# Kernel tuning notes

Measured on AMD Instinct MI355X. Metric: run time of the kernel, lower is better.

Reference implementation:

```python
import jax, jax.numpy as jnp
import numpy as np


def _logcumsumexp(x, axis):
    return jax.lax.associative_scan(jnp.logaddexp, x, axis=axis)


def _log_g(x):
    # log of g(x) = where(x>=0, x+0.5, sigmoid(x))
    return jnp.where(x >= 0, jnp.log(jax.nn.relu(x) + 0.5), -jax.nn.softplus(-x))


def _min_gru(x, Wz, bz, Wh, bh):
    # x: [B, S, D_in] -> h: [B, S, H]; log-space Heinsen parallel scan over S
    k = x @ Wz + bz                      # gate pre-activation
    log_z = -jax.nn.softplus(-k)         # log(sigmoid(k))  = log z
    log_coeffs = -jax.nn.softplus(k)     # log(1 - sigmoid(k))
    log_tilde_h = _log_g(x @ Wh + bh)    # log candidate hidden
    a_star = jnp.cumsum(log_coeffs, axis=1)
    log_h = a_star + _logcumsumexp(log_z + log_tilde_h - a_star, axis=1)
    return jnp.exp(log_h)


def setup_inputs() -> dict:
    key = jax.random.key(0)
    ks = jax.random.split(key, 7)
    B, S, D, H = 4, 4096, 1024, 1024
    s_in = 1.0 / np.sqrt(D)
    s_cat = 1.0 / np.sqrt(2 * H)
    return {
        "x": jax.random.normal(ks[0], (B, S, D), jnp.float32),
        "Wz_f": jax.random.normal(ks[1], (D, H), jnp.float32) * s_in,
        "bz_f": jnp.zeros((H,), jnp.float32),
        "Wh_f": jax.random.normal(ks[2], (D, H), jnp.float32) * s_in,
        "bh_f": jnp.zeros((H,), jnp.float32),
        "Wz_b": jax.random.normal(ks[3], (D, H), jnp.float32) * s_in,
        "bz_b": jnp.zeros((H,), jnp.float32),
        "Wh_b": jax.random.normal(ks[4], (D, H), jnp.float32) * s_in,
        "bh_b": jnp.zeros((H,), jnp.float32),
        "W_out": jax.random.normal(ks[5], (2 * H, H), jnp.float32) * s_cat,
        "b_out": jnp.zeros((H,), jnp.float32),
    }


def reference(x, Wz_f, bz_f, Wh_f, bh_f, Wz_b, bz_b, Wh_b, bh_b, W_out, b_out):
    x_rev = jnp.flip(x, axis=1)
    out_fwd = _min_gru(x, Wz_f, bz_f, Wh_f, bh_f)        # [B, S, H]
    out_bwd = _min_gru(x_rev, Wz_b, bz_b, Wh_b, bh_b)    # [B, S, H] (not re-flipped, per source)
    concat = jnp.concatenate([out_fwd, out_bwd], axis=2)  # [B, S, 2H]
    return concat @ W_out + b_out                         # [B, S, H]
```

## Files before the change

### kernel.cpp

```cpp
#include <hip/hip_runtime.h>
#include <stdint.h>

typedef __attribute__((ext_vector_type(8))) short bf16x8;
typedef __attribute__((ext_vector_type(4))) float f32x4;

#define SEQ 4096

__device__ __forceinline__ float bf2f(unsigned short u) {
  union { unsigned int i; float f; } v; v.i = ((unsigned int)u) << 16; return v.f;
}
__device__ __forceinline__ unsigned short f2bf(float f) {
  union { float f; unsigned int i; } v; v.f = f;
  unsigned int u = v.i;
  u = u + 0x7FFFu + ((u >> 16) & 1u);
  return (unsigned short)(u >> 16);
}
__device__ __forceinline__ float sigm(float x) { return 1.0f / (1.0f + __expf(-x)); }


__global__ void cvt_x_kernel(const float* __restrict__ in, unsigned short* __restrict__ out, int n8) {
  int i = blockIdx.x * blockDim.x + threadIdx.x;
  int stride = gridDim.x * blockDim.x;
  for (; i < n8; i += stride) {
    const float4* p = (const float4*)in + (size_t)i * 2;
    float4 a = p[0], b = p[1];
    union { unsigned short u[8]; uint4 v; } r;
    r.u[0] = f2bf(a.x); r.u[1] = f2bf(a.y); r.u[2] = f2bf(a.z); r.u[3] = f2bf(a.w);
    r.u[4] = f2bf(b.x); r.u[5] = f2bf(b.y); r.u[6] = f2bf(b.z); r.u[7] = f2bf(b.w);
    ((uint4*)out)[i] = r.v;
  }
}

__global__ void tconv32_kernel(const float* __restrict__ src, unsigned short* __restrict__ dst,
                               int K, int N) {
  __shared__ float t[32][33];
  int n0 = blockIdx.x * 32, k0 = blockIdx.y * 32;
  int tx = threadIdx.x & 31, ty = threadIdx.x >> 5;
#pragma unroll
  for (int i = 0; i < 32; i += 8)
    t[ty + i][tx] = src[(size_t)(k0 + ty + i) * N + n0 + tx];
  __syncthreads();
#pragma unroll
  for (int i = 0; i < 32; i += 8)
    dst[(size_t)(n0 + ty + i) * K + k0 + tx] = f2bf(t[tx][ty + i]);
}

__global__ void concat_bias_kernel(const float* b0, const float* b1, const float* b2,
                                   const float* b3, float* b4) {
  int i = blockIdx.x * 256 + threadIdx.x;
  const float* p = (i < 1024) ? b0 : (i < 2048) ? b1 : (i < 3072) ? b2 : b3;
  b4[i] = p[i & 1023];
}


template <int MODE>
__global__ __launch_bounds__(512, 2) void gemm256_kernel(
    const unsigned short* __restrict__ A, const unsigned short* __restrict__ BT,
    const float* __restrict__ bias, void* __restrict__ Cout, int K, int NT) {
  __shared__ unsigned short lds[32768];

  const int tid = threadIdx.x;
  const int lane = tid & 63;
  const int wv = tid >> 6;
  const int wm = wv >> 2;
  const int wn = wv & 3;
  const int lo = lane & 15, hi = lane >> 4;

  const int nwg = gridDim.x;
  const int bid = blockIdx.x;
  const int cpx = nwg >> 3;
  const int sw = (bid & 7) * cpx + (bid >> 3);
  const int mt = sw / NT, nt = sw - mt * NT;
  const int m0 = mt << 8, n0 = nt << 8;

  const int srow = tid >> 2;
  const int skb = (((tid & 3) ^ ((tid >> 3) & 3)) << 4);
  const unsigned short* pA0 = A + (size_t)(m0 + srow) * K + (skb >> 1);
  const unsigned short* pA1 = pA0 + (size_t)128 * K;
  const unsigned short* pB0 = BT + (size_t)(n0 + srow) * K + (skb >> 1);
  const unsigned short* pB1 = pB0 + (size_t)128 * K;
  const int dstBase = wv << 9;

#define GLL(SRC, DIDX)                                                                  \
  __builtin_amdgcn_global_load_lds((const __attribute__((address_space(1))) void*)(SRC), \
                                   (__attribute__((address_space(3))) void*)&lds[DIDX], \
                                   16, 0, 0)
#define STAGE(KT, BUF)                                   \
  do {                                                   \
    const int ko_ = (KT) << 5;                           \
    GLL(pA0 + ko_, (BUF) * 8192 + dstBase);              \
    GLL(pA1 + ko_, (BUF) * 8192 + 4096 + dstBase);       \
    GLL(pB0 + ko_, 16384 + (BUF) * 8192 + dstBase);      \
    GLL(pB1 + ko_, 16384 + (BUF) * 8192 + 4096 + dstBase); \
  } while (0)

  f32x4 acc[8][4];
#pragma unroll
  for (int i = 0; i < 8; ++i)
#pragma unroll
    for (int j = 0; j < 4; ++j) acc[i][j] = (f32x4){0.f, 0.f, 0.f, 0.f};

  const int swz = ((lo >> 1) & 3) << 4;
  const int kof = ((hi << 4) ^ swz) >> 1;
  const int aRow = wm * 128 + lo;
  const int bRow = wn * 64 + lo;

  const int nT = K >> 5;
  STAGE(0, 0);
  for (int kt = 0; kt < nT; ++kt) {
    const int buf = kt & 1;
    if (kt + 1 < nT) {
      STAGE(kt + 1, buf ^ 1);
      asm volatile("s_waitcnt vmcnt(4)" ::: "memory");
    } else {
      asm volatile("s_waitcnt vmcnt(0)" ::: "memory");
    }
    __builtin_amdgcn_s_barrier();
    const int aOff = buf * 8192;
    const int bOff = 16384 + buf * 8192;

    bf16x8 af[8];
#pragma unroll
    for (int mi = 0; mi < 8; ++mi)
      af[mi] = *(const bf16x8*)&lds[aOff + (aRow + mi * 16) * 32 + kof];
    bf16x8 b0 = *(const bf16x8*)&lds[bOff + (bRow + 0) * 32 + kof];
    bf16x8 b1 = *(const bf16x8*)&lds[bOff + (bRow + 16) * 32 + kof];
    __builtin_amdgcn_s_setprio(1);
#pragma unroll
    for (int mi = 0; mi < 8; ++mi) {
      acc[mi][0] = __builtin_amdgcn_mfma_f32_16x16x32_bf16(af[mi], b0, acc[mi][0], 0, 0, 0);
      acc[mi][1] = __builtin_amdgcn_mfma_f32_16x16x32_bf16(af[mi], b1, acc[mi][1], 0, 0, 0);
    }
    __builtin_amdgcn_s_setprio(0);
    __builtin_amdgcn_s_barrier();

    bf16x8 b2 = *(const bf16x8*)&lds[bOff + (bRow + 32) * 32 + kof];
    bf16x8 b3 = *(const bf16x8*)&lds[bOff + (bRow + 48) * 32 + kof];
    __builtin_amdgcn_s_setprio(1);
#pragma unroll
    for (int mi = 0; mi < 8; ++mi) {
      acc[mi][2] = __builtin_amdgcn_mfma_f32_16x16x32_bf16(af[mi], b2, acc[mi][2], 0, 0, 0);
      acc[mi][3] = __builtin_amdgcn_mfma_f32_16x16x32_bf16(af[mi], b3, acc[mi][3], 0, 0, 0);
    }
    __builtin_amdgcn_s_setprio(0);
    asm volatile("s_waitcnt lgkmcnt(0)" ::: "memory");
    __builtin_amdgcn_s_barrier();
  }
#undef STAGE
#undef GLL

#pragma unroll
  for (int mi = 0; mi < 8; ++mi) {
#pragma unroll
    for (int ni = 0; ni < 4; ++ni) {
      int col = n0 + wn * 64 + ni * 16 + lo;
      int rb = m0 + wm * 128 + mi * 16 + hi * 4;
      float bcol = bias[col];
      f32x4 v = acc[mi][ni];
      if (MODE == 0) {
        unsigned short* ACTp = (unsigned short*)Cout;
        bool isz = ((col >> 10) & 1) == 0;
#pragma unroll
        for (int r = 0; r < 4; ++r) {
          float x = v[r] + bcol;
          float res;
          if (isz) res = sigm(-x);
          else res = (x >= 0.f) ? (x + 0.5f) : sigm(x);
          ACTp[(size_t)(rb + r) * 4096 + col] = f2bf(res);
        }
      } else {
        float* Op = (float*)Cout;
#pragma unroll
        for (int r = 0; r < 4; ++r) Op[(size_t)(rb + r) * 1024 + col] = v[r] + bcol;
      }
    }
  }
}


__global__ __launch_bounds__(256) void scan_phase1_kernel(const unsigned short* __restrict__ ACT,
                                                          float* __restrict__ CHA,
                                                          float* __restrict__ CHB) {
  int tid = threadIdx.x;
  int cb = blockIdx.x & 3;
  int chunk = (blockIdx.x >> 2) & 31;
  int b = (blockIdx.x >> 7) & 3;
  int dir = (blockIdx.x >> 9) & 1;
  int c = cb * 256 + tid;
  int t0 = chunk * 128;
  size_t colA = (size_t)dir * 2048 + c;
  float Ap = 1.f, Bv = 0.f;
  for (int i = 0; i < 128; ++i) {
    int t = t0 + i;
    int s = dir ? (SEQ - 1 - t) : t;
    size_t base = ((size_t)b * SEQ + s) * 4096;
    float a = bf2f(ACT[base + colA]);
    float g = bf2f(ACT[base + colA + 1024]);
    Bv = a * Bv + (1.f - a) * g;
    Ap *= a;
  }
  size_t o = ((size_t)(dir * 4 + b) * 32 + chunk) * 1024 + c;
  CHA[o] = Ap;
  CHB[o] = Bv;
}

__global__ __launch_bounds__(256) void scan_phase2_kernel(const float* __restrict__ CHA,
                                                          const float* __restrict__ CHB,
                                                          float* __restrict__ HINIT) {
  int idx = blockIdx.x * 256 + threadIdx.x;
  int c = idx & 1023;
  int db = idx >> 10;
  float h = 0.f;
  for (int ck = 0; ck < 32; ++ck) {
    size_t o = ((size_t)db * 32 + ck) * 1024 + c;
    HINIT[o] = h;
    h = CHA[o] * h + CHB[o];
  }
}

__global__ __launch_bounds__(256) void scan_phase3_kernel(const unsigned short* __restrict__ ACT,
                                                          const float* __restrict__ HINIT,
                                                          unsigned short* __restrict__ HCAT) {
  int tid = threadIdx.x;
  int cb = blockIdx.x & 3;
  int chunk = (blockIdx.x >> 2) & 31;
  int b = (blockIdx.x >> 7) & 3;
  int dir = (blockIdx.x >> 9) & 1;
  int c = cb * 256 + tid;
  int t0 = chunk * 128;
  size_t colA = (size_t)dir * 2048 + c;
  float h = HINIT[((size_t)(dir * 4 + b) * 32 + chunk) * 1024 + c];
  for (int i = 0; i < 128; ++i) {
    int t = t0 + i;
    int s = dir ? (SEQ - 1 - t) : t;
    size_t base = ((size_t)b * SEQ + s) * 4096;
    float a = bf2f(ACT[base + colA]);
    float g = bf2f(ACT[base + colA + 1024]);
    h = a * h + (1.f - a) * g;
    HCAT[((size_t)b * SEQ + t) * 2048 + dir * 1024 + c] = f2bf(h);
  }
}


extern "C" void kernel_launch(void* const* d_in, const int* in_sizes, int n_in,
                              void* d_out, int out_size, void* d_ws, size_t ws_size,
                              hipStream_t stream) {
  (void)in_sizes; (void)n_in; (void)out_size; (void)ws_size;
  const float* x     = (const float*)d_in[0];
  const float* Wz_f  = (const float*)d_in[1];
  const float* bz_f  = (const float*)d_in[2];
  const float* Wh_f  = (const float*)d_in[3];
  const float* bh_f  = (const float*)d_in[4];
  const float* Wz_b  = (const float*)d_in[5];
  const float* bz_b  = (const float*)d_in[6];
  const float* Wh_b  = (const float*)d_in[7];
  const float* bh_b  = (const float*)d_in[8];
  const float* W_out = (const float*)d_in[9];
  const float* b_out = (const float*)d_in[10];

  char* ws = (char*)d_ws;
  size_t off = 0;
  auto alloc = [&](size_t bytes) {
    char* p = ws + off;
    off = (off + bytes + 255) & ~(size_t)255;
    return p;
  };
  const size_t M = 16384;
  unsigned short* xb    = (unsigned short*)alloc(M * 1024 * 2);
  unsigned short* WT4   = (unsigned short*)alloc(4096ull * 1024 * 2);
  unsigned short* WTout = (unsigned short*)alloc(1024ull * 2048 * 2);
  unsigned short* ACT   = (unsigned short*)alloc(M * 4096 * 2);
  unsigned short* HCAT  = (unsigned short*)alloc(M * 2048 * 2);
  float* CHA   = (float*)alloc(262144ull * 4);
  float* CHB   = (float*)alloc(262144ull * 4);
  float* HINIT = (float*)alloc(262144ull * 4);
  float* b4    = (float*)alloc(4096 * 4);

  cvt_x_kernel<<<2048, 256, 0, stream>>>(x, xb, (int)(M * 1024 / 8));

  tconv32_kernel<<<dim3(32, 32), 256, 0, stream>>>(Wz_f, WT4 + 0 * 1048576, 1024, 1024);
  tconv32_kernel<<<dim3(32, 32), 256, 0, stream>>>(Wh_f, WT4 + 1 * 1048576, 1024, 1024);
  tconv32_kernel<<<dim3(32, 32), 256, 0, stream>>>(Wz_b, WT4 + 2 * 1048576, 1024, 1024);
  tconv32_kernel<<<dim3(32, 32), 256, 0, stream>>>(Wh_b, WT4 + 3 * 1048576, 1024, 1024);
  tconv32_kernel<<<dim3(32, 64), 256, 0, stream>>>(W_out, WTout, 2048, 1024);
  concat_bias_kernel<<<16, 256, 0, stream>>>(bz_f, bh_f, bz_b, bh_b, b4);

  gemm256_kernel<0><<<1024, 512, 0, stream>>>(xb, WT4, b4, (void*)ACT, 1024, 16);

  scan_phase1_kernel<<<1024, 256, 0, stream>>>(ACT, CHA, CHB);
  scan_phase2_kernel<<<32, 256, 0, stream>>>(CHA, CHB, HINIT);
  scan_phase3_kernel<<<1024, 256, 0, stream>>>(ACT, HINIT, HCAT);

  gemm256_kernel<1><<<256, 512, 0, stream>>>(HCAT, WTout, b_out, d_out, 2048, 4);
}
```

Baseline: 337.8 us.

## Merge weight transposes, split gate GEMM with BK64 variant, vectorize scan kernels

The five weight-transpose launches become one 3D-grid launch. The first GEMM is split into two half-N launches: one keeps the original BK=32 kernel and the other uses a new BK=64 variant with a 128KB LDS double buffer. The scan phases 1 and 3 now process 4 channels per thread with vector loads and stores, and the chunk count goes from 32 to 64 with shorter chunks. This cuts launch overhead and uncoalesced narrow scan accesses. The 128KB LDS kernel limits occupancy to one block per CU, and splitting the GEMM leaves a partial wave at its tail.

```diff
diff --git a/kernel.cpp b/kernel.cpp
--- a/kernel.cpp
+++ b/kernel.cpp
@@ -3,6 +3,7 @@
 
 typedef __attribute__((ext_vector_type(8))) short bf16x8;
 typedef __attribute__((ext_vector_type(4))) float f32x4;
+typedef __attribute__((ext_vector_type(4))) unsigned short u16x4;
 
 #define SEQ 4096
 
@@ -31,14 +32,24 @@
   }
 }
 
-__global__ void tconv32_kernel(const float* __restrict__ src, unsigned short* __restrict__ dst,
-                               int K, int N) {
+__global__ void tconvb_kernel(const float* __restrict__ s0, const float* __restrict__ s1,
+                              const float* __restrict__ s2, const float* __restrict__ s3,
+                              const float* __restrict__ s4, unsigned short* __restrict__ WT4,
+                              unsigned short* __restrict__ WTout) {
   __shared__ float t[32][33];
-  int n0 = blockIdx.x * 32, k0 = blockIdx.y * 32;
+  int z = blockIdx.z;
+  const float* src; unsigned short* dst; int K, k0;
+  if (z < 4) {
+    src = (z == 0) ? s0 : (z == 1) ? s1 : (z == 2) ? s2 : s3;
+    dst = WT4 + (size_t)z * 1048576; K = 1024; k0 = blockIdx.y * 32;
+  } else {
+    src = s4; dst = WTout; K = 2048; k0 = blockIdx.y * 32 + (z - 4) * 1024;
+  }
+  int n0 = blockIdx.x * 32;
   int tx = threadIdx.x & 31, ty = threadIdx.x >> 5;
 #pragma unroll
   for (int i = 0; i < 32; i += 8)
-    t[ty + i][tx] = src[(size_t)(k0 + ty + i) * N + n0 + tx];
+    t[ty + i][tx] = src[(size_t)(k0 + ty + i) * 1024 + n0 + tx];
   __syncthreads();
 #pragma unroll
   for (int i = 0; i < 32; i += 8)
@@ -52,11 +63,42 @@
   b4[i] = p[i & 1023];
 }
 
+template <int MODE>
+__device__ __forceinline__ void gemm_epilogue(f32x4 (&acc)[8][4], const float* bias,
+                                              void* Cout, int m0, int n0, int wm, int wn,
+                                              int lo, int hi) {
+#pragma unroll
+  for (int mi = 0; mi < 8; ++mi) {
+#pragma unroll
+    for (int ni = 0; ni < 4; ++ni) {
+      int col = n0 + wn * 64 + ni * 16 + lo;
+      int rb = m0 + wm * 128 + mi * 16 + hi * 4;
+      float bcol = bias[col];
+      f32x4 v = acc[mi][ni];
+      if (MODE == 0) {
+        unsigned short* ACTp = (unsigned short*)Cout;
+        bool isz = ((col >> 10) & 1) == 0;
+#pragma unroll
+        for (int r = 0; r < 4; ++r) {
+          float x = v[r] + bcol;
+          float res;
+          if (isz) res = sigm(-x);
+          else res = (x >= 0.f) ? (x + 0.5f) : sigm(x);
+          ACTp[(size_t)(rb + r) * 4096 + col] = f2bf(res);
+        }
+      } else {
+        float* Op = (float*)Cout;
+#pragma unroll
+        for (int r = 0; r < 4; ++r) Op[(size_t)(rb + r) * 1024 + col] = v[r] + bcol;
+      }
+    }
+  }
+}
 
 template <int MODE>
 __global__ __launch_bounds__(512, 2) void gemm256_kernel(
     const unsigned short* __restrict__ A, const unsigned short* __restrict__ BT,
-    const float* __restrict__ bias, void* __restrict__ Cout, int K, int NT) {
+    const float* __restrict__ bias, void* __restrict__ Cout, int K, int NT, int ntOff) {
   __shared__ unsigned short lds[32768];
 
   const int tid = threadIdx.x;
@@ -71,7 +113,7 @@
   const int cpx = nwg >> 3;
   const int sw = (bid & 7) * cpx + (bid >> 3);
   const int mt = sw / NT, nt = sw - mt * NT;
-  const int m0 = mt << 8, n0 = nt << 8;
+  const int m0 = mt << 8, n0 = (nt + ntOff) << 8;
 
   const int srow = tid >> 2;
   const int skb = (((tid & 3) ^ ((tid >> 3) & 3)) << 4);
@@ -85,12 +127,12 @@
   __builtin_amdgcn_global_load_lds((const __attribute__((address_space(1))) void*)(SRC), \
                                    (__attribute__((address_space(3))) void*)&lds[DIDX], \
                                    16, 0, 0)
-#define STAGE(KT, BUF)                                   \
-  do {                                                   \
-    const int ko_ = (KT) << 5;                           \
-    GLL(pA0 + ko_, (BUF) * 8192 + dstBase);              \
-    GLL(pA1 + ko_, (BUF) * 8192 + 4096 + dstBase);       \
-    GLL(pB0 + ko_, 16384 + (BUF) * 8192 + dstBase);      \
+#define STAGE(KT, BUF)                                     \
+  do {                                                     \
+    const int ko_ = (KT) << 5;                             \
+    GLL(pA0 + ko_, (BUF) * 8192 + dstBase);                \
+    GLL(pA1 + ko_, (BUF) * 8192 + 4096 + dstBase);         \
+    GLL(pB0 + ko_, 16384 + (BUF) * 8192 + dstBase);        \
     GLL(pB1 + ko_, 16384 + (BUF) * 8192 + 4096 + dstBase); \
   } while (0)
 
@@ -148,60 +190,130 @@
   }
 #undef STAGE
 #undef GLL
-
-#pragma unroll
-  for (int mi = 0; mi < 8; ++mi) {
-#pragma unroll
-    for (int ni = 0; ni < 4; ++ni) {
-      int col = n0 + wn * 64 + ni * 16 + lo;
-      int rb = m0 + wm * 128 + mi * 16 + hi * 4;
-      float bcol = bias[col];
-      f32x4 v = acc[mi][ni];
-      if (MODE == 0) {
-        unsigned short* ACTp = (unsigned short*)Cout;
-        bool isz = ((col >> 10) & 1) == 0;
-#pragma unroll
-        for (int r = 0; r < 4; ++r) {
-          float x = v[r] + bcol;
-          float res;
-          if (isz) res = sigm(-x);
-          else res = (x >= 0.f) ? (x + 0.5f) : sigm(x);
-          ACTp[(size_t)(rb + r) * 4096 + col] = f2bf(res);
-        }
-      } else {
-        float* Op = (float*)Cout;
-#pragma unroll
-        for (int r = 0; r < 4; ++r) Op[(size_t)(rb + r) * 1024 + col] = v[r] + bcol;
-      }
-    }
-  }
-}
-
-
-__global__ __launch_bounds__(256) void scan_phase1_kernel(const unsigned short* __restrict__ ACT,
-                                                          float* __restrict__ CHA,
-                                                          float* __restrict__ CHB) {
-  int tid = threadIdx.x;
-  int cb = blockIdx.x & 3;
-  int chunk = (blockIdx.x >> 2) & 31;
-  int b = (blockIdx.x >> 7) & 3;
-  int dir = (blockIdx.x >> 9) & 1;
-  int c = cb * 256 + tid;
-  int t0 = chunk * 128;
-  size_t colA = (size_t)dir * 2048 + c;
-  float Ap = 1.f, Bv = 0.f;
-  for (int i = 0; i < 128; ++i) {
+  gemm_epilogue<MODE>(acc, bias, Cout, m0, n0, wm, wn, lo, hi);
+}
+
+template <int MODE>
+__global__ __launch_bounds__(512, 2) void gemm256b_kernel(
+    const unsigned short* __restrict__ A, const unsigned short* __restrict__ BT,
+    const float* __restrict__ bias, void* __restrict__ Cout, int K, int NT, int ntOff) {
+  __shared__ unsigned short lds[65536];
+
+  const int tid = threadIdx.x;
+  const int lane = tid & 63;
+  const int wv = tid >> 6;
+  const int wm = wv >> 2;
+  const int wn = wv & 3;
+  const int lo = lane & 15, hi = lane >> 4;
+
+  const int nwg = gridDim.x;
+  const int bid = blockIdx.x;
+  const int cpx = nwg >> 3;
+  const int sw = (bid & 7) * cpx + (bid >> 3);
+  const int mt = sw / NT, nt = sw - mt * NT;
+  const int m0 = mt << 8, n0 = (nt + ntOff) << 8;
+
+  const int srow = tid >> 3;
+  const int skb = (((tid & 7) ^ ((tid >> 3) & 7)) << 4);
+  const unsigned short* pA = A + (size_t)(m0 + srow) * K + (skb >> 1);
+  const unsigned short* pB = BT + (size_t)(n0 + srow) * K + (skb >> 1);
+  const int dstBase = wv << 9;
+
+#define GLLB(SRC, DIDX)                                                                 \
+  __builtin_amdgcn_global_load_lds((const __attribute__((address_space(1))) void*)(SRC), \
+                                   (__attribute__((address_space(3))) void*)&lds[DIDX], \
+                                   16, 0, 0)
+#define STAGEB(KT, BUF)                                          \
+  do {                                                           \
+    const int ko_ = (KT) << 6;                                   \
+    _Pragma("unroll")                                            \
+    for (int j = 0; j < 4; ++j) {                                \
+      GLLB(pA + (size_t)64 * j * K + ko_,                        \
+           (BUF) * 16384 + j * 4096 + dstBase);                  \
+      GLLB(pB + (size_t)64 * j * K + ko_,                        \
+           32768 + (BUF) * 16384 + j * 4096 + dstBase);          \
+    }                                                            \
+  } while (0)
+
+  f32x4 acc[8][4];
+#pragma unroll
+  for (int i = 0; i < 8; ++i)
+#pragma unroll
+    for (int j = 0; j < 4; ++j) acc[i][j] = (f32x4){0.f, 0.f, 0.f, 0.f};
+
+  const int swz8 = (lo & 7) << 4;
+  const int aRow = wm * 128 + lo;
+  const int bRow = wn * 64 + lo;
+
+  const int nT = K >> 6;
+  STAGEB(0, 0);
+  for (int kt = 0; kt < nT; ++kt) {
+    const int buf = kt & 1;
+    if (kt + 1 < nT) {
+      STAGEB(kt + 1, buf ^ 1);
+      asm volatile("s_waitcnt vmcnt(8)" ::: "memory");
+    } else {
+      asm volatile("s_waitcnt vmcnt(0)" ::: "memory");
+    }
+    __builtin_amdgcn_s_barrier();
+    const int aOff = buf * 16384;
+    const int bOff = 32768 + buf * 16384;
+
+#pragma unroll
+    for (int ks = 0; ks < 2; ++ks) {
+      const int kof = ((ks * 64 + hi * 16) ^ swz8) >> 1;
+      bf16x8 af[8], bf[4];
+#pragma unroll
+      for (int mi = 0; mi < 8; ++mi)
+        af[mi] = *(const bf16x8*)&lds[aOff + (aRow + mi * 16) * 64 + kof];
+#pragma unroll
+      for (int ni = 0; ni < 4; ++ni)
+        bf[ni] = *(const bf16x8*)&lds[bOff + (bRow + ni * 16) * 64 + kof];
+      __builtin_amdgcn_s_setprio(1);
+#pragma unroll
+      for (int mi = 0; mi < 8; ++mi)
+#pragma unroll
+        for (int ni = 0; ni < 4; ++ni)
+          acc[mi][ni] = __builtin_amdgcn_mfma_f32_16x16x32_bf16(af[mi], bf[ni],
+                                                                acc[mi][ni], 0, 0, 0);
+      __builtin_amdgcn_s_setprio(0);
+    }
+    asm volatile("s_waitcnt lgkmcnt(0)" ::: "memory");
+    __builtin_amdgcn_s_barrier();
+  }
+#undef STAGEB
+#undef GLLB
+  gemm_epilogue<MODE>(acc, bias, Cout, m0, n0, wm, wn, lo, hi);
+}
+
+
+__global__ __launch_bounds__(256) void scan1v_kernel(const unsigned short* __restrict__ ACT,
+                                                     float* __restrict__ CHA,
+                                                     float* __restrict__ CHB) {
+  int chunk = blockIdx.x & 63;
+  int b = (blockIdx.x >> 6) & 3;
+  int dir = blockIdx.x >> 8;
+  int c4 = threadIdx.x * 4;
+  size_t colA = (size_t)dir * 2048 + c4;
+  float Ap[4] = {1.f, 1.f, 1.f, 1.f};
+  float Bv[4] = {0.f, 0.f, 0.f, 0.f};
+  int t0 = chunk * 64;
+  for (int i = 0; i < 64; ++i) {
     int t = t0 + i;
     int s = dir ? (SEQ - 1 - t) : t;
-    size_t base = ((size_t)b * SEQ + s) * 4096;
-    float a = bf2f(ACT[base + colA]);
-    float g = bf2f(ACT[base + colA + 1024]);
-    Bv = a * Bv + (1.f - a) * g;
-    Ap *= a;
-  }
-  size_t o = ((size_t)(dir * 4 + b) * 32 + chunk) * 1024 + c;
-  CHA[o] = Ap;
-  CHB[o] = Bv;
+    size_t base = ((size_t)b * SEQ + s) * 4096 + colA;
+    u16x4 av = *(const u16x4*)&ACT[base];
+    u16x4 gv = *(const u16x4*)&ACT[base + 1024];
+#pragma unroll
+    for (int j = 0; j < 4; ++j) {
+      float a = bf2f(av[j]), g = bf2f(gv[j]);
+      Bv[j] = a * Bv[j] + (1.f - a) * g;
+      Ap[j] *= a;
+    }
+  }
+  size_t o = ((size_t)(dir * 4 + b) * 64 + chunk) * 1024 + c4;
+  *(float4*)&CHA[o] = (float4){Ap[0], Ap[1], Ap[2], Ap[3]};
+  *(float4*)&CHB[o] = (float4){Bv[0], Bv[1], Bv[2], Bv[3]};
 }
 
 __global__ __launch_bounds__(256) void scan_phase2_kernel(const float* __restrict__ CHA,
@@ -211,33 +323,38 @@
   int c = idx & 1023;
   int db = idx >> 10;
   float h = 0.f;
-  for (int ck = 0; ck < 32; ++ck) {
-    size_t o = ((size_t)db * 32 + ck) * 1024 + c;
+  for (int ck = 0; ck < 64; ++ck) {
+    size_t o = ((size_t)db * 64 + ck) * 1024 + c;
     HINIT[o] = h;
     h = CHA[o] * h + CHB[o];
   }
 }
 
-__global__ __launch_bounds__(256) void scan_phase3_kernel(const unsigned short* __restrict__ ACT,
-                                                          const float* __restrict__ HINIT,
-                                                          unsigned short* __restrict__ HCAT) {
-  int tid = threadIdx.x;
-  int cb = blockIdx.x & 3;
-  int chunk = (blockIdx.x >> 2) & 31;
-  int b = (blockIdx.x >> 7) & 3;
-  int dir = (blockIdx.x >> 9) & 1;
-  int c = cb * 256 + tid;
-  int t0 = chunk * 128;
-  size_t colA = (size_t)dir * 2048 + c;
-  float h = HINIT[((size_t)(dir * 4 + b) * 32 + chunk) * 1024 + c];
-  for (int i = 0; i < 128; ++i) {
+__global__ __launch_bounds__(256) void scan3v_kernel(const unsigned short* __restrict__ ACT,
+                                                     const float* __restrict__ HINIT,
+                                                     unsigned short* __restrict__ HCAT) {
+  int chunk = blockIdx.x & 63;
+  int b = (blockIdx.x >> 6) & 3;
+  int dir = blockIdx.x >> 8;
+  int c4 = threadIdx.x * 4;
+  size_t colA = (size_t)dir * 2048 + c4;
+  float4 h0 = *(const float4*)&HINIT[((size_t)(dir * 4 + b) * 64 + chunk) * 1024 + c4];
+  float h[4] = {h0.x, h0.y, h0.z, h0.w};
+  int t0 = chunk * 64;
+  for (int i = 0; i < 64; ++i) {
     int t = t0 + i;
     int s = dir ? (SEQ - 1 - t) : t;
-    size_t base = ((size_t)b * SEQ + s) * 4096;
-    float a = bf2f(ACT[base + colA]);
-    float g = bf2f(ACT[base + colA + 1024]);
-    h = a * h + (1.f - a) * g;
-    HCAT[((size_t)b * SEQ + t) * 2048 + dir * 1024 + c] = f2bf(h);
+    size_t base = ((size_t)b * SEQ + s) * 4096 + colA;
+    u16x4 av = *(const u16x4*)&ACT[base];
+    u16x4 gv = *(const u16x4*)&ACT[base + 1024];
+    u16x4 out;
+#pragma unroll
+    for (int j = 0; j < 4; ++j) {
+      float a = bf2f(av[j]), g = bf2f(gv[j]);
+      h[j] = a * h[j] + (1.f - a) * g;
+      out[j] = f2bf(h[j]);
+    }
+    *(u16x4*)&HCAT[((size_t)b * SEQ + t) * 2048 + dir * 1024 + c4] = out;
   }
 }
 
@@ -271,25 +388,22 @@
   unsigned short* WTout = (unsigned short*)alloc(1024ull * 2048 * 2);
   unsigned short* ACT   = (unsigned short*)alloc(M * 4096 * 2);
   unsigned short* HCAT  = (unsigned short*)alloc(M * 2048 * 2);
-  float* CHA   = (float*)alloc(262144ull * 4);
-  float* CHB   = (float*)alloc(262144ull * 4);
-  float* HINIT = (float*)alloc(262144ull * 4);
+  float* CHA   = (float*)alloc(524288ull * 4);
+  float* CHB   = (float*)alloc(524288ull * 4);
+  float* HINIT = (float*)alloc(524288ull * 4);
   float* b4    = (float*)alloc(4096 * 4);
 
   cvt_x_kernel<<<2048, 256, 0, stream>>>(x, xb, (int)(M * 1024 / 8));
 
-  tconv32_kernel<<<dim3(32, 32), 256, 0, stream>>>(Wz_f, WT4 + 0 * 1048576, 1024, 1024);
-  tconv32_kernel<<<dim3(32, 32), 256, 0, stream>>>(Wh_f, WT4 + 1 * 1048576, 1024, 1024);
-  tconv32_kernel<<<dim3(32, 32), 256, 0, stream>>>(Wz_b, WT4 + 2 * 1048576, 1024, 1024);
-  tconv32_kernel<<<dim3(32, 32), 256, 0, stream>>>(Wh_b, WT4 + 3 * 1048576, 1024, 1024);
-  tconv32_kernel<<<dim3(32, 64), 256, 0, stream>>>(W_out, WTout, 2048, 1024);
+  tconvb_kernel<<<dim3(32, 32, 6), 256, 0, stream>>>(Wz_f, Wh_f, Wz_b, Wh_b, W_out, WT4, WTout);
   concat_bias_kernel<<<16, 256, 0, stream>>>(bz_f, bh_f, bz_b, bh_b, b4);
 
-  gemm256_kernel<0><<<1024, 512, 0, stream>>>(xb, WT4, b4, (void*)ACT, 1024, 16);
-
-  scan_phase1_kernel<<<1024, 256, 0, stream>>>(ACT, CHA, CHB);
+  gemm256_kernel<0><<<512, 512, 0, stream>>>(xb, WT4, b4, (void*)ACT, 1024, 8, 0);
+  gemm256b_kernel<0><<<512, 512, 0, stream>>>(xb, WT4, b4, (void*)ACT, 1024, 8, 8);
+
+  scan1v_kernel<<<512, 256, 0, stream>>>(ACT, CHA, CHB);
   scan_phase2_kernel<<<32, 256, 0, stream>>>(CHA, CHB, HINIT);
-  scan_phase3_kernel<<<1024, 256, 0, stream>>>(ACT, HINIT, HCAT);
-
-  gemm256_kernel<1><<<256, 512, 0, stream>>>(HCAT, WTout, b_out, d_out, 2048, 4);
-}
+  scan3v_kernel<<<512, 256, 0, stream>>>(ACT, HINIT, HCAT);
+
+  gemm256_kernel<1><<<256, 512, 0, stream>>>(HCAT, WTout, b_out, d_out, 2048, 4, 0);
+}
```

New measurement: 463.2 us. 1.37x slower.
